# Performance work log

Measured on AMD Instinct MI355X. Metric: run time of the kernel, lower is better.

## Reference

```python
import jax, jax.numpy as jnp
import numpy as np

B, N, DIM, H, POS_DIM = 4, 1024, 256, 8, 16
DH = DIM // H          # 32, head dim
DP = DIM // 8          # 32, pos feature dim


def setup_inputs() -> dict:
    key = jax.random.key(0)
    ks = jax.random.split(key, 16)
    s = lambda k, shp, fan: jax.random.normal(k, shp, jnp.float32) / np.sqrt(fan)
    return {
        "x": jax.random.normal(ks[0], (B, N, DIM), jnp.float32),
        "deep_semantics": jax.random.normal(ks[1], (B, N, DIM), jnp.float32),
        "pos": jax.random.normal(ks[2], (B, N, POS_DIM), jnp.float32),
        "Wq": s(ks[3], (DIM, DIM), DIM),
        "Wk": s(ks[4], (DIM, DIM), DIM),
        "Wv": s(ks[5], (DIM, DIM), DIM),
        "Wo": s(ks[6], (DIM, DIM), DIM),
        "bo": jnp.zeros((DIM,), jnp.float32),
        "Wp1": s(ks[7], (POS_DIM, POS_DIM), POS_DIM),
        "bp1": jnp.zeros((POS_DIM,), jnp.float32),
        "Wp2": s(ks[8], (POS_DIM, DP), POS_DIM),
        "bp2": jnp.zeros((DP,), jnp.float32),
        "Wh": s(ks[9], (DP, H), DP),
        "bh": jnp.zeros((H,), jnp.float32),
        "gate": jnp.ones((H,), jnp.float32),
    }


def reference(x, deep_semantics, pos, Wq, Wk, Wv, Wo, bo,
              Wp1, bp1, Wp2, bp2, Wh, bh, gate):
    b, n, d = x.shape
    split = lambda t: t.reshape(b, n, H, DH).transpose(0, 2, 1, 3)  # [B,H,N,dh]
    q = split(x @ Wq)
    k = split(x @ Wk)
    v = split(x @ Wv)

    # qk branch
    scores = jnp.einsum('bhnd,bhmd->bhnm', q, k) / np.sqrt(DH)
    attn = jax.nn.softmax(scores, axis=-1)                          # [B,H,N,N]

    # positional branch: MLP on pos, pairwise diff, per-head logits
    p = jax.nn.relu(pos @ Wp1 + bp1) @ Wp2 + bp2                    # [B,N,DP]
    diff = p[:, :, None, :] - p[:, None, :, :]                      # [B,N,N,DP]
    pos_logits = (diff @ Wh + bh).transpose(0, 3, 1, 2)             # [B,H,N,N]
    pos_attn = jax.nn.softmax(pos_logits, axis=-1)

    # gated combination + renormalization
    g = jax.nn.sigmoid(gate)[None, :, None, None]
    a = (1.0 - g) * attn + g * pos_attn
    a = a / jnp.sum(a, axis=-1, keepdims=True)

    out = jnp.einsum('bhnm,bhmd->bhnd', a, v)
    out = out.transpose(0, 2, 1, 3).reshape(b, n, d)
    out = out @ Wo + bo
    return out
```

## Files before the change

kernel.cpp:

```cpp
#include <hip/hip_runtime.h>
#include <hip/hip_bf16.h>


constexpr int N_ = 1024, PD_ = 16;

typedef short  s8v  __attribute__((ext_vector_type(8)));
typedef float  f16v __attribute__((ext_vector_type(16)));
typedef unsigned u4v __attribute__((ext_vector_type(4)));

__device__ inline unsigned pkbf(float lo, float hi) {
  unsigned r;
  asm("v_cvt_pk_bf16_f32 %0, %1, %2" : "=v"(r) : "v"(lo), "v"(hi));
  return r;
}
__device__ inline short bf16r(float f) {
  unsigned u = __float_as_uint(f);
  u += 0x7fff + ((u >> 16) & 1);
  return (short)(u >> 16);
}
__device__ inline float bfu(short s) {
  return __uint_as_float(((unsigned)(unsigned short)s) << 16);
}

__global__ __launch_bounds__(256) void k_prep(
    const float* __restrict__ Wq, const float* __restrict__ Wk,
    const float* __restrict__ Wv, const float* __restrict__ Wo,
    const float* __restrict__ pos, const float* __restrict__ Wp1,
    const float* __restrict__ bp1, const float* __restrict__ Wp2,
    const float* __restrict__ bp2, const float* __restrict__ Wh,
    const float* __restrict__ x,
    short* __restrict__ Wtf, short* __restrict__ Wof, float* __restrict__ Ww,
    short* __restrict__ xf, float* __restrict__ pv)
{
  int bid = blockIdx.x;
  int tid = threadIdx.x;

  if (bid >= 96) {
    size_t idx = ((size_t)(bid - 96) * 256 + tid) * 8;
    int m = (int)(idx >> 8), k0 = (int)(idx & 255);
    const float4* p = (const float4*)(x + idx);
    float4 f0 = p[0], f1 = p[1];
    u4v o = { pkbf(f0.x, f0.y), pkbf(f0.z, f0.w), pkbf(f1.x, f1.y), pkbf(f1.z, f1.w) };
    size_t dst = ((size_t)((m >> 5) * 16 + (k0 >> 4))) * 512 + (m & 31) * 16 + (k0 & 15);
    *(u4v*)(xf + dst) = o;
    return;
  }

  if (bid < 64) {
    __shared__ float tile[64][65];
    int mat = bid >> 4, t = bid & 15;
    int k0t = (t >> 2) * 64, c0t = (t & 3) * 64;
    const float* W = mat == 0 ? Wq : mat == 1 ? Wk : mat == 2 ? Wv : Wo;
    float scale = (mat == 0) ? 0.2550348662f : 1.0f;
#pragma unroll
    for (int i = 0; i < 16; ++i) {
      int e = tid + i * 256;
      int kr = e >> 6, cc = e & 63;
      tile[kr][cc] = W[(size_t)(k0t + kr) * 256 + c0t + cc];
    }
    __syncthreads();
    short* dst = (mat == 3) ? Wof : (Wtf + mat * 65536);
#pragma unroll
    for (int i = 0; i < 16; ++i) {
      int e = tid + i * 256;
      int cr = e >> 6, kk = e & 63;
      int c = c0t + cr, k = k0t + kk;
      size_t a = ((size_t)((c >> 5) * 16 + (k >> 4))) * 512 + (c & 31) * 16 + (k & 15);
      dst[a] = bf16r(tile[kk][cr] * scale);
    }
    return;
  }

  __shared__ float sWp1[256], sbp1[16], sWp2[512], sbp2[32], sWhc[32];
  __shared__ float redm[4], reds[4];
  int bh = bid - 64;
  int b = bh >> 3, h = bh & 7;
  if (tid < 32) pv[bh * 32 + tid] = 0.0f;
  sWp1[tid] = Wp1[tid];
  sWp2[tid] = Wp2[tid];
  sWp2[tid + 256] = Wp2[tid + 256];
  if (tid < 16) sbp1[tid] = bp1[tid];
  if (tid < 32) { sbp2[tid] = bp2[tid]; sWhc[tid] = Wh[tid * 8 + h]; }
  __syncthreads();

  float a[4];
#pragma unroll
  for (int nn = 0; nn < 4; ++nn) {
    int n = nn * 256 + tid;
    const float* prow = pos + (size_t)((b << 10) + n) * PD_;
    float pr[16];
#pragma unroll
    for (int r = 0; r < 16; ++r) pr[r] = prow[r];
    float h1[16];
#pragma unroll
    for (int c = 0; c < 16; ++c) {
      float v = sbp1[c];
#pragma unroll
      for (int r = 0; r < 16; ++r) v = fmaf(pr[r], sWp1[r * 16 + c], v);
      h1[c] = fmaxf(v, 0.0f);
    }
    float s = 0.0f;
#pragma unroll
    for (int d = 0; d < 32; ++d) {
      float v = sbp2[d];
#pragma unroll
      for (int c = 0; c < 16; ++c) v = fmaf(h1[c], sWp2[c * 32 + d], v);
      s = fmaf(v, sWhc[d], s);
    }
    a[nn] = -s;
  }
  float m = fmaxf(fmaxf(a[0], a[1]), fmaxf(a[2], a[3]));
#pragma unroll
  for (int off = 32; off >= 1; off >>= 1) m = fmaxf(m, __shfl_xor(m, off));
  if ((tid & 63) == 0) redm[tid >> 6] = m;
  __syncthreads();
  float M = fmaxf(fmaxf(redm[0], redm[1]), fmaxf(redm[2], redm[3]));
  float e0 = __expf(a[0] - M), e1 = __expf(a[1] - M);
  float e2 = __expf(a[2] - M), e3 = __expf(a[3] - M);
  float su = e0 + e1 + e2 + e3;
#pragma unroll
  for (int off = 32; off >= 1; off >>= 1) su += __shfl_xor(su, off);
  if ((tid & 63) == 0) reds[tid >> 6] = su;
  __syncthreads();
  float inv = 1.0f / (reds[0] + reds[1] + reds[2] + reds[3]);
  float* wr = Ww + (size_t)bh * N_;
  wr[tid]        = e0 * inv;
  wr[tid + 256]  = e1 * inv;
  wr[tid + 512]  = e2 * inv;
  wr[tid + 768]  = e3 * inv;
}

__global__ __launch_bounds__(256) void k_qkv(
    const short* __restrict__ xf, const short* __restrict__ Wtf,
    const float* __restrict__ Ww,
    short* __restrict__ Qf, short* __restrict__ Kf, short* __restrict__ Vf,
    float* __restrict__ pv)
{
  int tid = threadIdx.x;
  int w = tid >> 6, l = tid & 63, H = l >> 5, li = l & 31;
  int bid = blockIdx.x;
  int cb = bid % 12, mb = bid / 12;
  int m0 = mb * 64 + (w & 1) * 32;
  int c0 = cb * 64 + (w >> 1) * 32;
  int mat = c0 >> 8, mc = c0 & 255;
  const short* Apf = xf + ((size_t)((m0 >> 5) * 16)) * 512 + li * 16 + 8 * H;
  const short* Bpf = Wtf + (size_t)mat * 65536
                   + ((size_t)((mc >> 5) * 16)) * 512 + li * 16 + 8 * H;
  f16v acc = {};
#pragma unroll
  for (int kc = 0; kc < 16; ++kc) {
    s8v af = *(const s8v*)(Apf + kc * 512);
    s8v bf = *(const s8v*)(Bpf + kc * 512);
    acc = __builtin_amdgcn_mfma_f32_32x32x16_bf16(af, bf, acc, 0, 0, 0);
  }
  int h = mc >> 5;
  int b = m0 >> 10, nb = m0 & 1023;
  int bh = b * 8 + h;
  if (mat < 2) {
    short* Dst = (mat == 0) ? Qf : Kf;
    size_t base = ((size_t)(bh * 2 + (li >> 4))) * 1024;
#pragma unroll
    for (int r = 0; r < 16; ++r) {
      int crow = (r & 3) + 8 * (r >> 2) + 4 * H;
      Dst[(base + nb + crow) * 16 + (li & 15)] = bf16r(acc[r]);
    }
  } else {
    int ks = nb >> 5;
#pragma unroll
    for (int q2 = 0; q2 < 4; ++q2) {
      uint2 val = make_uint2(pkbf(acc[q2 * 4 + 0], acc[q2 * 4 + 1]),
                             pkbf(acc[q2 * 4 + 2], acc[q2 * 4 + 3]));
      size_t addr = (((size_t)(bh * 32 + ks) * 2 + (q2 >> 1)) * 32 + li) * 16
                  + (q2 & 1) * 8 + 4 * H;
      *(uint2*)(Vf + addr) = val;
    }
    const float* wp = Ww + (size_t)bh * N_ + nb;
    float part = 0.0f;
#pragma unroll
    for (int r = 0; r < 16; ++r) {
      int crow = (r & 3) + 8 * (r >> 2) + 4 * H;
      part = fmaf(wp[crow], acc[r], part);
    }
    atomicAdd(&pv[bh * 32 + li], part);
  }
}

__global__ __launch_bounds__(512) void k_attn(
    const short* __restrict__ Qf, const short* __restrict__ Kf,
    const short* __restrict__ Vf, const float* __restrict__ pv,
    const float* __restrict__ gate,
    short* __restrict__ OHfh, short* __restrict__ OHfl)
{
  __shared__ float sml[8][32];
  __shared__ float sO[8][32][33];
  int tid = threadIdx.x;
  int w = tid >> 6, l = tid & 63, H = l >> 5, li = l & 31;
  int bid = blockIdx.x;
  int bh = (bid & 7) * 4 + (bid >> 8);
  int qb = (bid >> 3) & 31;
  int n0 = qb * 32;

  const short* Qpf = Qf + ((size_t)(bh * 2) * 1024 + n0 + li) * 16 + 8 * H;
  s8v qf0 = *(const s8v*)(Qpf);
  s8v qf1 = *(const s8v*)(Qpf + 16384);
  const short* Kbf = Kf + ((size_t)(bh * 2) * 1024 + li) * 16 + 8 * H;
  const short* Vbf = Vf + ((size_t)(bh * 32) * 2 * 32) * 16 + li * 16 + H * 8;

  f16v acc = {};
  float lsum = 0.0f;

#pragma unroll 2
  for (int ch = 0; ch < 4; ++ch) {
    int jb = w * 128 + ch * 32;
    int ks = jb >> 5;
    const short* Kp = Kbf + (size_t)jb * 16;
    s8v kf0 = *(const s8v*)(Kp);
    s8v kf1 = *(const s8v*)(Kp + 16384);
    const short* Vp = Vbf + (size_t)(ks * 2) * 512;
    s8v vf0 = *(const s8v*)(Vp);
    s8v vf1 = *(const s8v*)(Vp + 512);

    f16v S = {};
    S = __builtin_amdgcn_mfma_f32_32x32x16_bf16(kf0, qf0, S, 0, 0, 0);
    S = __builtin_amdgcn_mfma_f32_32x32x16_bf16(kf1, qf1, S, 0, 0, 0);

    float p[16];
#pragma unroll
    for (int r = 0; r < 16; ++r) {
      p[r] = __builtin_amdgcn_exp2f(S[r]);
      lsum += p[r];
    }

    unsigned a0 = pkbf(p[0], p[1]),  a1 = pkbf(p[2], p[3]);
    unsigned b0 = pkbf(p[4], p[5]),  b1 = pkbf(p[6], p[7]);
    unsigned c0 = pkbf(p[8], p[9]),  c1 = pkbf(p[10], p[11]);
    unsigned d0 = pkbf(p[12], p[13]), d1 = pkbf(p[14], p[15]);
    unsigned sa0 = __shfl_xor(a0, 32), sa1 = __shfl_xor(a1, 32);
    unsigned sb0 = __shfl_xor(b0, 32), sb1 = __shfl_xor(b1, 32);
    unsigned sc0 = __shfl_xor(c0, 32), sc1 = __shfl_xor(c1, 32);
    unsigned sd0 = __shfl_xor(d0, 32), sd1 = __shfl_xor(d1, 32);
    u4v t0 = { H ? sb0 : a0, H ? sb1 : a1, H ? b0 : sa0, H ? b1 : sa1 };
    u4v t1 = { H ? sd0 : c0, H ? sd1 : c1, H ? d0 : sc0, H ? d1 : sc1 };

    acc = __builtin_amdgcn_mfma_f32_32x32x16_bf16(vf0, __builtin_bit_cast(s8v, t0), acc, 0, 0, 0);
    acc = __builtin_amdgcn_mfma_f32_32x32x16_bf16(vf1, __builtin_bit_cast(s8v, t1), acc, 0, 0, 0);
  }

  lsum += __shfl_xor(lsum, 32);
  if (H == 0) sml[w][li] = lsum;
#pragma unroll
  for (int r = 0; r < 16; ++r) {
    int d = (r & 3) + 8 * (r >> 2) + 4 * H;
    sO[w][d][li] = acc[r];
  }
  __syncthreads();

  if (tid < 256) {
    int i = tid >> 3, dq = (tid & 7) * 4;
    float L = sml[0][i] + sml[1][i] + sml[2][i] + sml[3][i]
            + sml[4][i] + sml[5][i] + sml[6][i] + sml[7][i];
    int b = bh >> 3, h = bh & 7;
    float gh = 1.0f / (1.0f + __expf(-gate[h]));
    float invL = (1.0f - gh) / L;
    const float4 pvv = *(const float4*)(pv + bh * 32 + dq);
    float o[4];
#pragma unroll
    for (int q = 0; q < 4; ++q) {
      o[q] = (sO[0][dq + q][i] + sO[1][dq + q][i] + sO[2][dq + q][i] + sO[3][dq + q][i]
            + sO[4][dq + q][i] + sO[5][dq + q][i] + sO[6][dq + q][i] + sO[7][dq + q][i]) * invL;
    }
    o[0] += gh * pvv.x; o[1] += gh * pvv.y; o[2] += gh * pvv.z; o[3] += gh * pvv.w;
    float hi[4], lo[4];
#pragma unroll
    for (int q = 0; q < 4; ++q) {
      hi[q] = bfu(bf16r(o[q]));
      lo[q] = o[q] - hi[q];
    }
    int kc = h * 2 + (dq >> 4);
    int rem = dq & 15;
    size_t addr = ((size_t)((b * 32 + qb) * 16 + kc)) * 512 + i * 16 + rem;
    *(uint2*)(OHfh + addr) = make_uint2(pkbf(hi[0], hi[1]), pkbf(hi[2], hi[3]));
    *(uint2*)(OHfl + addr) = make_uint2(pkbf(lo[0], lo[1]), pkbf(lo[2], lo[3]));
  }
}

__global__ __launch_bounds__(256) void k_out(
    const short* __restrict__ OHfh, const short* __restrict__ OHfl,
    const short* __restrict__ Wof, const float* __restrict__ bo,
    float* __restrict__ out)
{
  int tid = threadIdx.x;
  int w = tid >> 6, l = tid & 63, H = l >> 5, li = l & 31;
  int bid = blockIdx.x;
  int m0 = (bid >> 2) * 64 + (w & 1) * 32;
  int c0 = (bid & 3) * 64 + (w >> 1) * 32;
  const short* Ahf = OHfh + ((size_t)((m0 >> 5) * 16)) * 512 + li * 16 + 8 * H;
  const short* Alf = OHfl + ((size_t)((m0 >> 5) * 16)) * 512 + li * 16 + 8 * H;
  const short* Bpf = Wof + ((size_t)((c0 >> 5) * 16)) * 512 + li * 16 + 8 * H;
  f16v acc = {};
#pragma unroll
  for (int kc = 0; kc < 16; ++kc) {
    s8v bf = *(const s8v*)(Bpf + kc * 512);
    s8v ah = *(const s8v*)(Ahf + kc * 512);
    s8v al = *(const s8v*)(Alf + kc * 512);
    acc = __builtin_amdgcn_mfma_f32_32x32x16_bf16(ah, bf, acc, 0, 0, 0);
    acc = __builtin_amdgcn_mfma_f32_32x32x16_bf16(al, bf, acc, 0, 0, 0);
  }
  float bias = bo[c0 + li];
#pragma unroll
  for (int r = 0; r < 16; ++r) {
    int crow = (r & 3) + 8 * (r >> 2) + 4 * H;
    out[(size_t)(m0 + crow) * 256 + c0 + li] = acc[r] + bias;
  }
}

extern "C" void kernel_launch(void* const* d_in, const int* in_sizes, int n_in,
                              void* d_out, int out_size, void* d_ws, size_t ws_size,
                              hipStream_t stream) {
  const float* x    = (const float*)d_in[0];
  const float* pos  = (const float*)d_in[2];
  const float* Wq   = (const float*)d_in[3];
  const float* Wk   = (const float*)d_in[4];
  const float* Wv   = (const float*)d_in[5];
  const float* Wo   = (const float*)d_in[6];
  const float* bo   = (const float*)d_in[7];
  const float* Wp1  = (const float*)d_in[8];
  const float* bp1  = (const float*)d_in[9];
  const float* Wp2  = (const float*)d_in[10];
  const float* bp2  = (const float*)d_in[11];
  const float* Wh   = (const float*)d_in[12];
  const float* gate = (const float*)d_in[14];
  float* out = (float*)d_out;

  char* base = (char*)d_ws;
  short* Qf   = (short*)(base);
  short* Kf   = (short*)(base + (2u << 20));
  short* Vf   = (short*)(base + (4u << 20));
  short* OHfh = (short*)(base + (6u << 20));
  short* OHfl = (short*)(base + (8u << 20));
  short* xf   = (short*)(base + (10u << 20));
  short* Wtf  = (short*)(base + (12u << 20));
  short* Wof  = (short*)(base + (12u << 20) + (384u << 10));
  float* Ww   = (float*)(base + (12u << 20) + (512u << 10));
  float* pv   = (float*)(base + (12u << 20) + (640u << 10));

  k_prep<<<608,  256, 0, stream>>>(Wq, Wk, Wv, Wo, pos, Wp1, bp1, Wp2, bp2, Wh,
                                   x, Wtf, Wof, Ww, xf, pv);
  k_qkv <<<768,  256, 0, stream>>>(xf, Wtf, Ww, Qf, Kf, Vf, pv);
  k_attn<<<1024, 512, 0, stream>>>(Qf, Kf, Vf, pv, gate, OHfh, OHfl);
  k_out <<<256,  256, 0, stream>>>(OHfh, OHfl, Wof, bo, out);
}
```

Baseline: 43.76 us.

## Replicate bf16 weights per XCD and remap blocks for L2 locality

The prep kernel now writes eight copies of the transformed weight matrices, one per XCD. The QKV, x-conversion and output-projection kernels remap block IDs so each XCD (bid & 7) works on a contiguous slice of rows and reads its own weight copy. The aim is to keep weight and activation reads inside each XCD's private L2 instead of crossing dies. The cost is eight times as many weight writes in the prep kernel and a larger workspace.

```diff
diff --git a/kernel.cpp b/kernel.cpp
--- a/kernel.cpp
+++ b/kernel.cpp
@@ -3,6 +3,8 @@
 
 
 constexpr int N_ = 1024, PD_ = 16;
+constexpr int WTF_CP = 196608;
+constexpr int WOF_CP = 65536;
 
 typedef short  s8v  __attribute__((ext_vector_type(8)));
 typedef float  f16v __attribute__((ext_vector_type(16)));
@@ -36,10 +38,13 @@
   int tid = threadIdx.x;
 
   if (bid >= 96) {
-    size_t idx = ((size_t)(bid - 96) * 256 + tid) * 8;
+    int p = bid - 96;
+    int xcd = p & 7, j = p >> 3;
+    int t = 128 * (xcd >> 1) + 64 * (xcd & 1) + j;
+    size_t idx = ((size_t)t * 256 + tid) * 8;
     int m = (int)(idx >> 8), k0 = (int)(idx & 255);
-    const float4* p = (const float4*)(x + idx);
-    float4 f0 = p[0], f1 = p[1];
+    const float4* pp = (const float4*)(x + idx);
+    float4 f0 = pp[0], f1 = pp[1];
     u4v o = { pkbf(f0.x, f0.y), pkbf(f0.z, f0.w), pkbf(f1.x, f1.y), pkbf(f1.z, f1.w) };
     size_t dst = ((size_t)((m >> 5) * 16 + (k0 >> 4))) * 512 + (m & 31) * 16 + (k0 & 15);
     *(u4v*)(xf + dst) = o;
@@ -59,14 +64,21 @@
       tile[kr][cc] = W[(size_t)(k0t + kr) * 256 + c0t + cc];
     }
     __syncthreads();
-    short* dst = (mat == 3) ? Wof : (Wtf + mat * 65536);
 #pragma unroll
     for (int i = 0; i < 16; ++i) {
       int e = tid + i * 256;
       int cr = e >> 6, kk = e & 63;
       int c = c0t + cr, k = k0t + kk;
       size_t a = ((size_t)((c >> 5) * 16 + (k >> 4))) * 512 + (c & 31) * 16 + (k & 15);
-      dst[a] = bf16r(tile[kk][cr] * scale);
+      short v = bf16r(tile[kk][cr] * scale);
+      if (mat == 3) {
+#pragma unroll
+        for (int cp = 0; cp < 8; ++cp) Wof[(size_t)cp * WOF_CP + a] = v;
+      } else {
+#pragma unroll
+        for (int cp = 0; cp < 8; ++cp)
+          Wtf[(size_t)cp * WTF_CP + mat * 65536 + a] = v;
+      }
     }
     return;
   }
@@ -139,12 +151,16 @@
   int tid = threadIdx.x;
   int w = tid >> 6, l = tid & 63, H = l >> 5, li = l & 31;
   int bid = blockIdx.x;
-  int cb = bid % 12, mb = bid / 12;
+  int xcd = bid & 7, j = bid >> 3;
+  int bq = xcd >> 1, hb = xcd & 1;
+  int cbi = j / 16, mbi = j % 16;
+  int cb = (cbi >> 1) * 4 + 2 * hb + (cbi & 1);
+  int mb = bq * 16 + mbi;
   int m0 = mb * 64 + (w & 1) * 32;
   int c0 = cb * 64 + (w >> 1) * 32;
   int mat = c0 >> 8, mc = c0 & 255;
   const short* Apf = xf + ((size_t)((m0 >> 5) * 16)) * 512 + li * 16 + 8 * H;
-  const short* Bpf = Wtf + (size_t)mat * 65536
+  const short* Bpf = Wtf + (size_t)xcd * WTF_CP + (size_t)mat * 65536
                    + ((size_t)((mc >> 5) * 16)) * 512 + li * 16 + 8 * H;
   f16v acc = {};
 #pragma unroll
@@ -292,11 +308,15 @@
   int tid = threadIdx.x;
   int w = tid >> 6, l = tid & 63, H = l >> 5, li = l & 31;
   int bid = blockIdx.x;
-  int m0 = (bid >> 2) * 64 + (w & 1) * 32;
-  int c0 = (bid & 3) * 64 + (w >> 1) * 32;
+  int xcd = bid & 7, j = bid >> 3;
+  int bq = xcd >> 1, e = xcd & 1;
+  int o_ = bq * 64 + e * 32 + j;
+  int m0 = (o_ >> 2) * 64 + (w & 1) * 32;
+  int c0 = (o_ & 3) * 64 + (w >> 1) * 32;
   const short* Ahf = OHfh + ((size_t)((m0 >> 5) * 16)) * 512 + li * 16 + 8 * H;
   const short* Alf = OHfl + ((size_t)((m0 >> 5) * 16)) * 512 + li * 16 + 8 * H;
-  const short* Bpf = Wof + ((size_t)((c0 >> 5) * 16)) * 512 + li * 16 + 8 * H;
+  const short* Bpf = Wof + (size_t)xcd * WOF_CP
+                   + ((size_t)((c0 >> 5) * 16)) * 512 + li * 16 + 8 * H;
   f16v acc = {};
 #pragma unroll
   for (int kc = 0; kc < 16; ++kc) {
@@ -340,9 +360,9 @@
   short* OHfl = (short*)(base + (8u << 20));
   short* xf   = (short*)(base + (10u << 20));
   short* Wtf  = (short*)(base + (12u << 20));
-  short* Wof  = (short*)(base + (12u << 20) + (384u << 10));
-  float* Ww   = (float*)(base + (12u << 20) + (512u << 10));
-  float* pv   = (float*)(base + (12u << 20) + (640u << 10));
+  short* Wof  = (short*)(base + (15u << 20));
+  float* Ww   = (float*)(base + (16u << 20));
+  float* pv   = (float*)(base + (16u << 20) + (128u << 10));
 
   k_prep<<<608,  256, 0, stream>>>(Wq, Wk, Wv, Wo, pos, Wp1, bp1, Wp2, bp2, Wh,
                                    x, Wtf, Wof, Ww, xf, pv);
```

Result: faster. 41.08 us (-6.1%).
